# Performance work log

Measured on AMD Instinct MI355X. Metric: run time of the kernel, lower is better.

Reference implementation:

```python
import jax, jax.numpy as jnp
import numpy as np

B, S, D, K = 4, 8192, 512, 20


def setup_inputs() -> dict:
    key = jax.random.key(0)
    k1, k2, k3, k4 = jax.random.split(key, 4)
    std = 0.02  # _init_weights: normal(0, 0.02/sqrt(layer_idx+1)), layer_idx=0
    return {
        "x": jax.random.normal(k1, (B, S, D), dtype=jnp.float32),
        "positions": jax.random.normal(k2, (K, D), dtype=jnp.float32) * 0.2,
        "log_scales": jnp.log(1.0 + 0.5 * jax.random.uniform(k3, (K,), dtype=jnp.float32)),
        "amplitudes": 1.2 + 0.3 * jax.random.uniform(k4, (K,), dtype=jnp.float32),
        "w_v": jax.random.normal(jax.random.fold_in(key, 10), (D, D), dtype=jnp.float32) * std,
        "w_o": jax.random.normal(jax.random.fold_in(key, 11), (D, D), dtype=jnp.float32) * std,
    }


def reference(x, positions, log_scales, amplitudes, w_v, w_o):
    # Gaussian-splat RBF attention (token -> splat -> token routing).
    scales = jnp.exp(log_scales)  # [K]
    # squared distances ||x - c||^2 via expansion (avoids [B,S,K,D] tensor)
    x2 = jnp.sum(x * x, axis=-1, keepdims=True)           # [B,S,1]
    c2 = jnp.sum(positions * positions, axis=-1)          # [K]
    xc = jnp.einsum('bsd,kd->bsk', x, positions)          # [B,S,K]
    d2 = jnp.maximum(x2 - 2.0 * xc + c2, 0.0)             # [B,S,K]
    gauss = amplitudes * jnp.exp(-0.5 * d2 / (scales * scales))  # [B,S,K]
    attn = gauss / (jnp.sum(gauss, axis=-1, keepdims=True) + 1e-8)  # per-token normalize
    v = jnp.einsum('bsd,ed->bse', x, w_v)                 # token_value_proj (no bias)
    splat_states = jnp.einsum('bsk,bsd->bkd', attn, v)    # gather token values at splats
    out = jnp.einsum('bsk,bkd->bsd', attn, splat_states)  # scatter back to tokens
    return jnp.einsum('bsd,ed->bse', out, w_o)            # output_proj (dropout=eval identity)
```

## Files before the change

### kernel.cpp

```cpp
#include <hip/hip_runtime.h>
#include <hip/hip_bf16.h>

#define BB 4
#define SS 8192
#define DD 512
#define KK 20
#define GG 8
#define BKD (BB * KK * DD)

__device__ __forceinline__ float dot4(float4 a, float4 b) {
  return a.x * b.x + a.y * b.y + a.z * b.z + a.w * b.w;
}

__global__ void k0_params(const float* __restrict__ pos,
                          const float* __restrict__ log_scales,
                          const float* __restrict__ amps,
                          float* __restrict__ params) {
  int k = blockIdx.x;
  int lane = threadIdx.x;
  float acc = 0.f;
  for (int d = lane; d < DD; d += 64) { float p = pos[k * DD + d]; acc += p * p; }
#pragma unroll
  for (int off = 32; off > 0; off >>= 1) acc += __shfl_xor(acc, off);
  if (lane == 0) {
    params[k] = acc;
    float s = __expf(log_scales[k]);
    params[KK + k] = 0.5f / (s * s);
    params[2 * KK + k] = amps[k];
  }
}

__global__ __launch_bounds__(256) void kA_attn(
    const float* __restrict__ x, const float* __restrict__ pos,
    const float* __restrict__ params, float* __restrict__ attn_g) {
  __shared__ float pos_s[KK * DD];
  __shared__ float prm_s[3 * KK];
  int tid = threadIdx.x;
  for (int i = tid; i < KK * DD / 4; i += 256)
    ((float4*)pos_s)[i] = ((const float4*)pos)[i];
  if (tid < 3 * KK) prm_s[tid] = params[tid];
  __syncthreads();

  int b = blockIdx.x >> 7;
  int c = blockIdx.x & 127;
  size_t row0 = (size_t)b * SS + (size_t)c * 64;
  int q = tid >> 4;
  int dsub = tid & 15;

  const float* xq = x + (row0 + q) * DD;

  float acc[4][KK];
  float x2[4];
#pragma unroll
  for (int r = 0; r < 4; ++r) {
    x2[r] = 0.f;
#pragma unroll
    for (int k = 0; k < KK; ++k) acc[r][k] = 0.f;
  }

#pragma unroll 2
  for (int j = 0; j < 8; ++j) {
    int d0 = j * 64 + dsub * 4;
    float4 xv[4];
#pragma unroll
    for (int r = 0; r < 4; ++r) xv[r] = *(const float4*)(xq + (size_t)(r * 16) * DD + d0);
#pragma unroll
    for (int r = 0; r < 4; ++r) x2[r] += dot4(xv[r], xv[r]);
#pragma unroll
    for (int k = 0; k < KK; ++k) {
      float4 p = *(const float4*)(pos_s + k * DD + d0);
#pragma unroll
      for (int r = 0; r < 4; ++r) acc[r][k] += dot4(xv[r], p);
    }
  }

#pragma unroll
  for (int r = 0; r < 4; ++r) {
#pragma unroll
    for (int m = 1; m <= 8; m <<= 1) x2[r] += __shfl_xor(x2[r], m);
#pragma unroll
    for (int k = 0; k < KK; ++k) {
#pragma unroll
      for (int m = 1; m <= 8; m <<= 1) acc[r][k] += __shfl_xor(acc[r][k], m);
    }
  }

  if (dsub == 0) {
#pragma unroll
    for (int r = 0; r < 4; ++r) {
      float gg[KK];
      float sum = 0.f;
#pragma unroll
      for (int k = 0; k < KK; ++k) {
        float d2 = fmaxf(x2[r] - 2.f * acc[r][k] + prm_s[k], 0.f);
        gg[k] = prm_s[2 * KK + k] * __expf(-prm_s[KK + k] * d2);
        sum += gg[k];
      }
      float inv = 1.f / (sum + 1e-8f);
      float* ar = attn_g + (row0 + q + r * 16) * KK;
#pragma unroll
      for (int k = 0; k < KK; ++k) ar[k] = gg[k] * inv;
    }
  }
}

__global__ __launch_bounds__(256) void kB_scatter(
    const float* __restrict__ x, const float* __restrict__ attn,
    float* __restrict__ Mpart, int tpc) {
  int t = threadIdx.x;
  int c = blockIdx.x;
  int b = blockIdx.y;
  int cpb = gridDim.x;
  size_t row0 = (size_t)b * SS + (size_t)c * tpc;

  float2 Ml[KK];
#pragma unroll
  for (int k = 0; k < KK; ++k) Ml[k] = make_float2(0.f, 0.f);

  const float* xb = x + row0 * DD + 2 * t;
  const float* ab = attn + row0 * KK;
  for (int s = 0; s < tpc; ++s) {
    float2 xv = *(const float2*)(xb + (size_t)s * DD);
    const float4* ar4 = (const float4*)(ab + s * KK);
#pragma unroll
    for (int kk = 0; kk < KK / 4; ++kk) {
      float4 a4 = ar4[kk];
      Ml[4 * kk + 0].x += a4.x * xv.x; Ml[4 * kk + 0].y += a4.x * xv.y;
      Ml[4 * kk + 1].x += a4.y * xv.x; Ml[4 * kk + 1].y += a4.y * xv.y;
      Ml[4 * kk + 2].x += a4.z * xv.x; Ml[4 * kk + 2].y += a4.z * xv.y;
      Ml[4 * kk + 3].x += a4.w * xv.x; Ml[4 * kk + 3].y += a4.w * xv.y;
    }
  }
  float* mp = Mpart + ((size_t)b * cpb + c) * KK * DD + 2 * t;
#pragma unroll
  for (int k = 0; k < KK; ++k) *(float2*)(mp + (size_t)k * DD) = Ml[k];
}

__global__ __launch_bounds__(256) void kC1_reduce(
    const float* __restrict__ Mpart, float* __restrict__ red8,
    int cpb, int cpg) {
  int idx = blockIdx.x * 256 + threadIdx.x;
  int g = idx / BKD;
  int rem = idx - g * BKD;
  int b = rem / (KK * DD);
  int kd = rem - b * (KK * DD);
  const float* p = Mpart + ((size_t)b * cpb + (size_t)g * cpg) * KK * DD + kd;
  float acc = 0.f;
#pragma unroll 8
  for (int c = 0; c < cpg; ++c) acc += p[(size_t)c * KK * DD];
  red8[idx] = acc;
}

__global__ __launch_bounds__(256) void kP_gemv(
    const float* __restrict__ in, const float* __restrict__ W,
    float* __restrict__ out, int mode) {
  __shared__ float m_s[DD];
  int tid = threadIdx.x;
  int bk = blockIdx.x;
  int et = blockIdx.y;

  for (int i = tid; i < DD; i += 256) {
    float a;
    if (mode == 0) {
      const float* p = in + (size_t)bk * DD + i;
      a = 0.f;
#pragma unroll
      for (int g = 0; g < GG; ++g) a += p[(size_t)g * BKD];
    } else {
      a = in[(size_t)bk * DD + i];
    }
    m_s[i] = a;
  }
  __syncthreads();

  int wave = tid >> 6;
  int lane = tid & 63;
  float4 ma = ((const float4*)m_s)[lane];
  float4 mb = ((const float4*)m_s)[64 + lane];

#pragma unroll 4
  for (int rr = 0; rr < 16; ++rr) {
    int e = et * 64 + wave * 16 + rr;
    const float4* wrow = (const float4*)(W + (size_t)e * DD);
    float p = dot4(wrow[lane], ma) + dot4(wrow[64 + lane], mb);
#pragma unroll
    for (int m = 1; m <= 32; m <<= 1) p += __shfl_xor(p, m);
    if (lane == 0) out[(size_t)bk * DD + e] = p;
  }
}

__global__ __launch_bounds__(256) void k5_gather(
    const float* __restrict__ attn, const float* __restrict__ ws2,
    float* __restrict__ out) {
  int tid = threadIdx.x;
  int b = blockIdx.x >> 9;
  int sc = blockIdx.x & 511;
  size_t s0 = (size_t)sc * 16;
  int tr = tid >> 7;
  int e4 = tid & 127;

  float4 w[KK];
  const float* wb = ws2 + (size_t)b * KK * DD + e4 * 4;
#pragma unroll
  for (int k = 0; k < KK; ++k) w[k] = *(const float4*)(wb + (size_t)k * DD);

  size_t rowA = (size_t)b * SS + s0 + tr;
  const float* ar = attn + rowA * KK;
  float* orow = out + rowA * DD + e4 * 4;

#pragma unroll 2
  for (int i = 0; i < 8; ++i) {
    const float4* a4 = (const float4*)(ar + (size_t)2 * i * KK);
    float4 A = a4[0], Bv = a4[1], C = a4[2], Dv = a4[3], E = a4[4];
    float4 o = make_float4(0.f, 0.f, 0.f, 0.f);
#define ACC(av, kbase) \
    o.x += av * w[kbase].x; o.y += av * w[kbase].y; \
    o.z += av * w[kbase].z; o.w += av * w[kbase].w;
    ACC(A.x, 0)  ACC(A.y, 1)  ACC(A.z, 2)  ACC(A.w, 3)
    ACC(Bv.x, 4) ACC(Bv.y, 5) ACC(Bv.z, 6) ACC(Bv.w, 7)
    ACC(C.x, 8)  ACC(C.y, 9)  ACC(C.z, 10) ACC(C.w, 11)
    ACC(Dv.x, 12) ACC(Dv.y, 13) ACC(Dv.z, 14) ACC(Dv.w, 15)
    ACC(E.x, 16) ACC(E.y, 17) ACC(E.z, 18) ACC(E.w, 19)
#undef ACC
    *(float4*)(orow + (size_t)2 * i * DD) = o;
  }
}

extern "C" void kernel_launch(void* const* d_in, const int* in_sizes, int n_in,
                              void* d_out, int out_size, void* d_ws, size_t ws_size,
                              hipStream_t stream) {
  const float* x   = (const float*)d_in[0];
  const float* pos = (const float*)d_in[1];
  const float* ls  = (const float*)d_in[2];
  const float* am  = (const float*)d_in[3];
  const float* w_v = (const float*)d_in[4];
  const float* w_o = (const float*)d_in[5];
  float* out = (float*)d_out;

  float* ws     = (float*)d_ws;
  float* attn   = ws;
  float* ws2    = attn + (size_t)BB * SS * KK;
  float* ssb    = ws2 + (size_t)BB * KK * DD;
  float* params = ssb + (size_t)BB * KK * DD;
  float* red8   = params + 64;
  float* Mpart  = red8 + (size_t)GG * BKD;

  size_t head_f = (size_t)BB * SS * KK + 2 * (size_t)BB * KK * DD + 64 + (size_t)GG * BKD;
  int cpb = 128, tpc = 64;
  size_t need = (head_f + (size_t)BB * cpb * KK * DD) * sizeof(float);
  if (ws_size < need) { cpb = 64; tpc = 128; }
  int cpg = cpb / GG;

  k0_params<<<KK, 64, 0, stream>>>(pos, ls, am, params);
  kA_attn<<<512, 256, 0, stream>>>(x, pos, params, attn);
  kB_scatter<<<dim3(cpb, BB), 256, 0, stream>>>(x, attn, Mpart, tpc);
  kC1_reduce<<<(GG * BKD) / 256, 256, 0, stream>>>(Mpart, red8, cpb, cpg);
  kP_gemv<<<dim3(BB * KK, 8), 256, 0, stream>>>(red8, w_v, ssb, 0);
  kP_gemv<<<dim3(BB * KK, 8), 256, 0, stream>>>(ssb, w_o, ws2, 1);
  k5_gather<<<2048, 256, 0, stream>>>(attn, ws2, out);
}
```

Measured before the change: 256.9 us.

## Split attention kernel over splat halves and defer normalization to consumers

The attention kernel now runs on a 2D grid, with each block handling 10 of the 20 splats. This halves shared memory and per-thread accumulators so occupancy can rise and more blocks are launched. Each half writes unnormalized gaussians, staged through shared memory for coalesced stores, plus a partial sum. The scatter and gather kernels then apply the reciprocal of the summed partials. The scatter kernel also gets more chunks (256) so it has more parallelism, at the cost of a larger partial buffer to reduce. The trade-off is that x is read twice in the attention stage and extra reciprocal work is done downstream.

```diff
diff --git a/kernel.cpp b/kernel.cpp
--- a/kernel.cpp
+++ b/kernel.cpp
@@ -5,6 +5,7 @@
 #define SS 8192
 #define DD 512
 #define KK 20
+#define KH 10
 #define GG 8
 #define BKD (BB * KK * DD)
 
@@ -30,15 +31,23 @@
   }
 }
 
-__global__ __launch_bounds__(256) void kA_attn(
+__global__ __launch_bounds__(256) void kA_gauss(
     const float* __restrict__ x, const float* __restrict__ pos,
-    const float* __restrict__ params, float* __restrict__ attn_g) {
-  __shared__ float pos_s[KK * DD];
-  __shared__ float prm_s[3 * KK];
+    const float* __restrict__ params, float* __restrict__ gbuf,
+    float* __restrict__ gsum) {
+  __shared__ float pos_s[KH * DD];
+  __shared__ float g_s[64 * KH];
+  __shared__ float prm_s[3 * KH];
   int tid = threadIdx.x;
-  for (int i = tid; i < KK * DD / 4; i += 256)
-    ((float4*)pos_s)[i] = ((const float4*)pos)[i];
-  if (tid < 3 * KK) prm_s[tid] = params[tid];
+  int kh = blockIdx.y;
+
+  for (int i = tid; i < KH * DD / 4; i += 256)
+    ((float4*)pos_s)[i] = ((const float4*)(pos + kh * KH * DD))[i];
+  if (tid < KH) {
+    prm_s[tid]          = params[kh * KH + tid];
+    prm_s[KH + tid]     = params[KK + kh * KH + tid];
+    prm_s[2 * KH + tid] = params[2 * KK + kh * KH + tid];
+  }
   __syncthreads();
 
   int b = blockIdx.x >> 7;
@@ -49,13 +58,13 @@
 
   const float* xq = x + (row0 + q) * DD;
 
-  float acc[4][KK];
+  float acc[4][KH];
   float x2[4];
 #pragma unroll
   for (int r = 0; r < 4; ++r) {
     x2[r] = 0.f;
 #pragma unroll
-    for (int k = 0; k < KK; ++k) acc[r][k] = 0.f;
+    for (int k = 0; k < KH; ++k) acc[r][k] = 0.f;
   }
 
 #pragma unroll 2
@@ -67,7 +76,7 @@
 #pragma unroll
     for (int r = 0; r < 4; ++r) x2[r] += dot4(xv[r], xv[r]);
 #pragma unroll
-    for (int k = 0; k < KK; ++k) {
+    for (int k = 0; k < KH; ++k) {
       float4 p = *(const float4*)(pos_s + k * DD + d0);
 #pragma unroll
       for (int r = 0; r < 4; ++r) acc[r][k] += dot4(xv[r], p);
@@ -79,7 +88,7 @@
 #pragma unroll
     for (int m = 1; m <= 8; m <<= 1) x2[r] += __shfl_xor(x2[r], m);
 #pragma unroll
-    for (int k = 0; k < KK; ++k) {
+    for (int k = 0; k < KH; ++k) {
 #pragma unroll
       for (int m = 1; m <= 8; m <<= 1) acc[r][k] += __shfl_xor(acc[r][k], m);
     }
@@ -88,25 +97,29 @@
   if (dsub == 0) {
 #pragma unroll
     for (int r = 0; r < 4; ++r) {
-      float gg[KK];
+      int tok = q + r * 16;
       float sum = 0.f;
 #pragma unroll
-      for (int k = 0; k < KK; ++k) {
+      for (int k = 0; k < KH; ++k) {
         float d2 = fmaxf(x2[r] - 2.f * acc[r][k] + prm_s[k], 0.f);
-        gg[k] = prm_s[2 * KK + k] * __expf(-prm_s[KK + k] * d2);
-        sum += gg[k];
+        float g = prm_s[2 * KH + k] * __expf(-prm_s[KH + k] * d2);
+        g_s[tok * KH + k] = g;
+        sum += g;
       }
-      float inv = 1.f / (sum + 1e-8f);
-      float* ar = attn_g + (row0 + q + r * 16) * KK;
-#pragma unroll
-      for (int k = 0; k < KK; ++k) ar[k] = gg[k] * inv;
-    }
+      gsum[(row0 + tok) * 2 + kh] = sum;
+    }
+  }
+  __syncthreads();
+
+  for (int i = tid; i < 64 * KH; i += 256) {
+    int tok = i / KH, kl = i - tok * KH;
+    gbuf[(row0 + tok) * KK + kh * KH + kl] = g_s[i];
   }
 }
 
 __global__ __launch_bounds__(256) void kB_scatter(
-    const float* __restrict__ x, const float* __restrict__ attn,
-    float* __restrict__ Mpart, int tpc) {
+    const float* __restrict__ x, const float* __restrict__ gbuf,
+    const float* __restrict__ gsum, float* __restrict__ Mpart, int tpc) {
   int t = threadIdx.x;
   int c = blockIdx.x;
   int b = blockIdx.y;
@@ -118,9 +131,13 @@
   for (int k = 0; k < KK; ++k) Ml[k] = make_float2(0.f, 0.f);
 
   const float* xb = x + row0 * DD + 2 * t;
-  const float* ab = attn + row0 * KK;
+  const float* ab = gbuf + row0 * KK;
+  const float* sb = gsum + row0 * 2;
   for (int s = 0; s < tpc; ++s) {
+    float2 sv = *(const float2*)(sb + 2 * s);
+    float inv = 1.f / (sv.x + sv.y + 1e-8f);
     float2 xv = *(const float2*)(xb + (size_t)s * DD);
+    xv.x *= inv; xv.y *= inv;
     const float4* ar4 = (const float4*)(ab + s * KK);
 #pragma unroll
     for (int kk = 0; kk < KK / 4; ++kk) {
@@ -190,8 +207,8 @@
 }
 
 __global__ __launch_bounds__(256) void k5_gather(
-    const float* __restrict__ attn, const float* __restrict__ ws2,
-    float* __restrict__ out) {
+    const float* __restrict__ gbuf, const float* __restrict__ gsum,
+    const float* __restrict__ ws2, float* __restrict__ out) {
   int tid = threadIdx.x;
   int b = blockIdx.x >> 9;
   int sc = blockIdx.x & 511;
@@ -205,12 +222,15 @@
   for (int k = 0; k < KK; ++k) w[k] = *(const float4*)(wb + (size_t)k * DD);
 
   size_t rowA = (size_t)b * SS + s0 + tr;
-  const float* ar = attn + rowA * KK;
+  const float* ar = gbuf + rowA * KK;
+  const float* sr = gsum + rowA * 2;
   float* orow = out + rowA * DD + e4 * 4;
 
 #pragma unroll 2
   for (int i = 0; i < 8; ++i) {
     const float4* a4 = (const float4*)(ar + (size_t)2 * i * KK);
+    float2 sv = *(const float2*)(sr + (size_t)4 * i);
+    float inv = 1.f / (sv.x + sv.y + 1e-8f);
     float4 A = a4[0], Bv = a4[1], C = a4[2], Dv = a4[3], E = a4[4];
     float4 o = make_float4(0.f, 0.f, 0.f, 0.f);
 #define ACC(av, kbase) \
@@ -222,6 +242,7 @@
     ACC(Dv.x, 12) ACC(Dv.y, 13) ACC(Dv.z, 14) ACC(Dv.w, 15)
     ACC(E.x, 16) ACC(E.y, 17) ACC(E.z, 18) ACC(E.w, 19)
 #undef ACC
+    o.x *= inv; o.y *= inv; o.z *= inv; o.w *= inv;
     *(float4*)(orow + (size_t)2 * i * DD) = o;
   }
 }
@@ -238,24 +259,28 @@
   float* out = (float*)d_out;
 
   float* ws     = (float*)d_ws;
-  float* attn   = ws;
-  float* ws2    = attn + (size_t)BB * SS * KK;
+  float* gbuf   = ws;
+  float* gsum   = gbuf + (size_t)BB * SS * KK;
+  float* ws2    = gsum + (size_t)BB * SS * 2;
   float* ssb    = ws2 + (size_t)BB * KK * DD;
   float* params = ssb + (size_t)BB * KK * DD;
   float* red8   = params + 64;
   float* Mpart  = red8 + (size_t)GG * BKD;
 
-  size_t head_f = (size_t)BB * SS * KK + 2 * (size_t)BB * KK * DD + 64 + (size_t)GG * BKD;
-  int cpb = 128, tpc = 64;
+  size_t head_f = (size_t)BB * SS * KK + (size_t)BB * SS * 2 +
+                  2 * (size_t)BB * KK * DD + 64 + (size_t)GG * BKD;
+  int cpb = 256;
   size_t need = (head_f + (size_t)BB * cpb * KK * DD) * sizeof(float);
-  if (ws_size < need) { cpb = 64; tpc = 128; }
+  if (ws_size < need) { cpb = 128; need = (head_f + (size_t)BB * cpb * KK * DD) * sizeof(float); }
+  if (ws_size < need) { cpb = 64; }
+  int tpc = SS / cpb;
   int cpg = cpb / GG;
 
   k0_params<<<KK, 64, 0, stream>>>(pos, ls, am, params);
-  kA_attn<<<512, 256, 0, stream>>>(x, pos, params, attn);
-  kB_scatter<<<dim3(cpb, BB), 256, 0, stream>>>(x, attn, Mpart, tpc);
+  kA_gauss<<<dim3(512, 2), 256, 0, stream>>>(x, pos, params, gbuf, gsum);
+  kB_scatter<<<dim3(cpb, BB), 256, 0, stream>>>(x, gbuf, gsum, Mpart, tpc);
   kC1_reduce<<<(GG * BKD) / 256, 256, 0, stream>>>(Mpart, red8, cpb, cpg);
   kP_gemv<<<dim3(BB * KK, 8), 256, 0, stream>>>(red8, w_v, ssb, 0);
   kP_gemv<<<dim3(BB * KK, 8), 256, 0, stream>>>(ssb, w_o, ws2, 1);
-  k5_gather<<<2048, 256, 0, stream>>>(attn, ws2, out);
-}
+  k5_gather<<<2048, 256, 0, stream>>>(gbuf, gsum, ws2, out);
+}
```

Measured after the change: 239.4 us. 6.8% less time.

## Defer softmax normalization, shrink attention blocks, and raise scatter chunk count

Applied to the files above, without the earlier changes.

The Gaussian kernel now handles 16 rows per block with one row per 16-thread group. It reads positions directly from global memory instead of staging them in LDS, and stores unnormalized weights plus a per-row sum with vectorized stores. The normalization is deferred into the scatter kernel, which scales x, and the gather kernel, which scales the output. The scatter kernel uses 256 chunks per batch when workspace allows. The aim is more blocks and occupancy in the attention stage and more parallelism in the scatter stage, at the cost of extra divides, more global position loads and a larger partial-sum reduction.

```diff
diff --git a/kernel.cpp b/kernel.cpp
--- a/kernel.cpp
+++ b/kernel.cpp
@@ -30,83 +30,69 @@
   }
 }
 
-__global__ __launch_bounds__(256) void kA_attn(
+__global__ __launch_bounds__(256, 6) void kA_gauss(
     const float* __restrict__ x, const float* __restrict__ pos,
-    const float* __restrict__ params, float* __restrict__ attn_g) {
-  __shared__ float pos_s[KK * DD];
+    const float* __restrict__ params, float* __restrict__ gbuf,
+    float* __restrict__ gsum) {
   __shared__ float prm_s[3 * KK];
   int tid = threadIdx.x;
-  for (int i = tid; i < KK * DD / 4; i += 256)
-    ((float4*)pos_s)[i] = ((const float4*)pos)[i];
   if (tid < 3 * KK) prm_s[tid] = params[tid];
   __syncthreads();
 
-  int b = blockIdx.x >> 7;
-  int c = blockIdx.x & 127;
-  size_t row0 = (size_t)b * SS + (size_t)c * 64;
-  int q = tid >> 4;
+  int g = tid >> 4;
   int dsub = tid & 15;
-
-  const float* xq = x + (row0 + q) * DD;
-
-  float acc[4][KK];
-  float x2[4];
-#pragma unroll
-  for (int r = 0; r < 4; ++r) {
-    x2[r] = 0.f;
-#pragma unroll
-    for (int k = 0; k < KK; ++k) acc[r][k] = 0.f;
-  }
+  int blk = blockIdx.x;
+  int b = blk >> 9;
+  int c = blk & 511;
+  size_t row = (size_t)b * SS + (size_t)c * 16 + g;
+  const float* xr = x + row * DD;
+
+  float acc[KK];
+  float x2 = 0.f;
+#pragma unroll
+  for (int k = 0; k < KK; ++k) acc[k] = 0.f;
 
 #pragma unroll 2
   for (int j = 0; j < 8; ++j) {
     int d0 = j * 64 + dsub * 4;
-    float4 xv[4];
-#pragma unroll
-    for (int r = 0; r < 4; ++r) xv[r] = *(const float4*)(xq + (size_t)(r * 16) * DD + d0);
-#pragma unroll
-    for (int r = 0; r < 4; ++r) x2[r] += dot4(xv[r], xv[r]);
+    float4 xv = *(const float4*)(xr + d0);
+    x2 += dot4(xv, xv);
 #pragma unroll
     for (int k = 0; k < KK; ++k) {
-      float4 p = *(const float4*)(pos_s + k * DD + d0);
-#pragma unroll
-      for (int r = 0; r < 4; ++r) acc[r][k] += dot4(xv[r], p);
-    }
-  }
-
-#pragma unroll
-  for (int r = 0; r < 4; ++r) {
-#pragma unroll
-    for (int m = 1; m <= 8; m <<= 1) x2[r] += __shfl_xor(x2[r], m);
+      float4 p = *(const float4*)(pos + k * DD + d0);
+      acc[k] += dot4(xv, p);
+    }
+  }
+
+#pragma unroll
+  for (int m = 1; m <= 8; m <<= 1) x2 += __shfl_xor(x2, m);
+#pragma unroll
+  for (int k = 0; k < KK; ++k) {
+#pragma unroll
+    for (int m = 1; m <= 8; m <<= 1) acc[k] += __shfl_xor(acc[k], m);
+  }
+
+  if (dsub == 0) {
+    float gg[KK];
+    float sum = 0.f;
 #pragma unroll
     for (int k = 0; k < KK; ++k) {
-#pragma unroll
-      for (int m = 1; m <= 8; m <<= 1) acc[r][k] += __shfl_xor(acc[r][k], m);
-    }
-  }
-
-  if (dsub == 0) {
-#pragma unroll
-    for (int r = 0; r < 4; ++r) {
-      float gg[KK];
-      float sum = 0.f;
-#pragma unroll
-      for (int k = 0; k < KK; ++k) {
-        float d2 = fmaxf(x2[r] - 2.f * acc[r][k] + prm_s[k], 0.f);
-        gg[k] = prm_s[2 * KK + k] * __expf(-prm_s[KK + k] * d2);
-        sum += gg[k];
-      }
-      float inv = 1.f / (sum + 1e-8f);
-      float* ar = attn_g + (row0 + q + r * 16) * KK;
-#pragma unroll
-      for (int k = 0; k < KK; ++k) ar[k] = gg[k] * inv;
-    }
+      float d2 = fmaxf(x2 - 2.f * acc[k] + prm_s[k], 0.f);
+      gg[k] = prm_s[2 * KK + k] * __expf(-prm_s[KK + k] * d2);
+      sum += gg[k];
+    }
+    float* gr = gbuf + row * KK;
+#pragma unroll
+    for (int kq = 0; kq < 5; ++kq)
+      *(float4*)(gr + 4 * kq) =
+          make_float4(gg[4 * kq], gg[4 * kq + 1], gg[4 * kq + 2], gg[4 * kq + 3]);
+    gsum[row] = sum;
   }
 }
 
 __global__ __launch_bounds__(256) void kB_scatter(
-    const float* __restrict__ x, const float* __restrict__ attn,
-    float* __restrict__ Mpart, int tpc) {
+    const float* __restrict__ x, const float* __restrict__ gbuf,
+    const float* __restrict__ gsum, float* __restrict__ Mpart, int tpc) {
   int t = threadIdx.x;
   int c = blockIdx.x;
   int b = blockIdx.y;
@@ -118,9 +104,12 @@
   for (int k = 0; k < KK; ++k) Ml[k] = make_float2(0.f, 0.f);
 
   const float* xb = x + row0 * DD + 2 * t;
-  const float* ab = attn + row0 * KK;
+  const float* ab = gbuf + row0 * KK;
+  const float* sb = gsum + row0;
   for (int s = 0; s < tpc; ++s) {
+    float inv = 1.f / (sb[s] + 1e-8f);
     float2 xv = *(const float2*)(xb + (size_t)s * DD);
+    xv.x *= inv; xv.y *= inv;
     const float4* ar4 = (const float4*)(ab + s * KK);
 #pragma unroll
     for (int kk = 0; kk < KK / 4; ++kk) {
@@ -190,8 +179,8 @@
 }
 
 __global__ __launch_bounds__(256) void k5_gather(
-    const float* __restrict__ attn, const float* __restrict__ ws2,
-    float* __restrict__ out) {
+    const float* __restrict__ gbuf, const float* __restrict__ gsum,
+    const float* __restrict__ ws2, float* __restrict__ out) {
   int tid = threadIdx.x;
   int b = blockIdx.x >> 9;
   int sc = blockIdx.x & 511;
@@ -205,12 +194,14 @@
   for (int k = 0; k < KK; ++k) w[k] = *(const float4*)(wb + (size_t)k * DD);
 
   size_t rowA = (size_t)b * SS + s0 + tr;
-  const float* ar = attn + rowA * KK;
+  const float* ar = gbuf + rowA * KK;
+  const float* sr = gsum + rowA;
   float* orow = out + rowA * DD + e4 * 4;
 
 #pragma unroll 2
   for (int i = 0; i < 8; ++i) {
     const float4* a4 = (const float4*)(ar + (size_t)2 * i * KK);
+    float inv = 1.f / (sr[(size_t)2 * i] + 1e-8f);
     float4 A = a4[0], Bv = a4[1], C = a4[2], Dv = a4[3], E = a4[4];
     float4 o = make_float4(0.f, 0.f, 0.f, 0.f);
 #define ACC(av, kbase) \
@@ -222,6 +213,7 @@
     ACC(Dv.x, 12) ACC(Dv.y, 13) ACC(Dv.z, 14) ACC(Dv.w, 15)
     ACC(E.x, 16) ACC(E.y, 17) ACC(E.z, 18) ACC(E.w, 19)
 #undef ACC
+    o.x *= inv; o.y *= inv; o.z *= inv; o.w *= inv;
     *(float4*)(orow + (size_t)2 * i * DD) = o;
   }
 }
@@ -238,24 +230,28 @@
   float* out = (float*)d_out;
 
   float* ws     = (float*)d_ws;
-  float* attn   = ws;
-  float* ws2    = attn + (size_t)BB * SS * KK;
+  float* gbuf   = ws;
+  float* gsum   = gbuf + (size_t)BB * SS * KK;
+  float* ws2    = gsum + (size_t)BB * SS;
   float* ssb    = ws2 + (size_t)BB * KK * DD;
   float* params = ssb + (size_t)BB * KK * DD;
   float* red8   = params + 64;
   float* Mpart  = red8 + (size_t)GG * BKD;
 
-  size_t head_f = (size_t)BB * SS * KK + 2 * (size_t)BB * KK * DD + 64 + (size_t)GG * BKD;
-  int cpb = 128, tpc = 64;
+  size_t head_f = (size_t)BB * SS * KK + (size_t)BB * SS +
+                  2 * (size_t)BB * KK * DD + 64 + (size_t)GG * BKD;
+  int cpb = 256;
   size_t need = (head_f + (size_t)BB * cpb * KK * DD) * sizeof(float);
-  if (ws_size < need) { cpb = 64; tpc = 128; }
+  if (ws_size < need) { cpb = 128; need = (head_f + (size_t)BB * cpb * KK * DD) * sizeof(float); }
+  if (ws_size < need) { cpb = 64; }
+  int tpc = SS / cpb;
   int cpg = cpb / GG;
 
   k0_params<<<KK, 64, 0, stream>>>(pos, ls, am, params);
-  kA_attn<<<512, 256, 0, stream>>>(x, pos, params, attn);
-  kB_scatter<<<dim3(cpb, BB), 256, 0, stream>>>(x, attn, Mpart, tpc);
+  kA_gauss<<<BB * SS / 16, 256, 0, stream>>>(x, pos, params, gbuf, gsum);
+  kB_scatter<<<dim3(cpb, BB), 256, 0, stream>>>(x, gbuf, gsum, Mpart, tpc);
   kC1_reduce<<<(GG * BKD) / 256, 256, 0, stream>>>(Mpart, red8, cpb, cpg);
   kP_gemv<<<dim3(BB * KK, 8), 256, 0, stream>>>(red8, w_v, ssb, 0);
   kP_gemv<<<dim3(BB * KK, 8), 256, 0, stream>>>(ssb, w_o, ws2, 1);
-  k5_gather<<<2048, 256, 0, stream>>>(attn, ws2, out);
-}
+  k5_gather<<<2048, 256, 0, stream>>>(gbuf, gsum, ws2, out);
+}
```

Result: no change. 257.8 us (+0.4%).
